# Kernel tuning notes

Hardware: AMD Instinct MI355X
Metric: run time of the kernel (lower is better)

## Reference

```python
import jax, jax.numpy as jnp
import numpy as np

B, S, D, H = 2, 2048, 1024, 16
DK = D // H  # 64
THETA = 10000.0


def setup_inputs() -> dict:
    key = jax.random.key(0)
    ks = jax.random.split(key, 5)
    std = float(np.sqrt(2.0 / (D + D)))
    x = jax.random.normal(ks[0], (B, S, D), dtype=jnp.float32)
    q_proj = jax.random.normal(ks[1], (D, D), dtype=jnp.float32) * std
    k_proj = jax.random.normal(ks[2], (D, D), dtype=jnp.float32) * std
    v_proj = jax.random.normal(ks[3], (D, D), dtype=jnp.float32) * std
    o_proj = jax.random.normal(ks[4], (D, D), dtype=jnp.float32) * std
    token_positions = jnp.arange(S, dtype=jnp.int32).reshape(1, S)
    return {"x": x, "token_positions": token_positions,
            "q_proj": q_proj, "k_proj": k_proj, "v_proj": v_proj, "o_proj": o_proj}


def _rope(t, pos):
    # t: [B, H, S, DK]; pos: [S]. Equivalent to multiplying by the block-diagonal
    # rotation matrix R[pos] in the source (interleaved 2x2 rotations).
    inv_freq = 1.0 / (THETA ** (2.0 * jnp.arange(DK // 2, dtype=jnp.float32) / DK))
    ang = pos.astype(jnp.float32)[:, None] * inv_freq[None, :]  # [S, DK/2]
    c, s = jnp.cos(ang), jnp.sin(ang)
    t0, t1 = t[..., 0::2], t[..., 1::2]
    out0 = c * t0 - s * t1
    out1 = s * t0 + c * t1
    return jnp.stack([out0, out1], axis=-1).reshape(t.shape)


def reference(x, token_positions, q_proj, k_proj, v_proj, o_proj):
    def split_heads(t):  # [B,S,D] -> [B,H,S,DK]
        return t.reshape(B, S, H, DK).transpose(0, 2, 1, 3)

    q = split_heads(jnp.einsum('bsd,ed->bse', x, q_proj))
    k = split_heads(jnp.einsum('bsd,ed->bse', x, k_proj))
    v = split_heads(jnp.einsum('bsd,ed->bse', x, v_proj))

    pos = token_positions[0]
    q = _rope(q, pos)
    k = _rope(k, pos)

    scores = jnp.einsum('bhqd,bhkd->bhqk', q, k) / jnp.sqrt(jnp.float32(DK))
    causal = jnp.tril(jnp.ones((S, S), dtype=bool))
    scores = jnp.where(causal, scores, -jnp.inf)

    # Faithful to source softmax: subtract the GLOBAL max (x.max()), then row-normalize.
    p = jnp.exp(scores - jnp.max(scores))
    p = p / jnp.sum(p, axis=-1, keepdims=True)

    attn = jnp.einsum('bhqk,bhkd->bhqd', p, v)
    attn = attn.transpose(0, 2, 1, 3).reshape(B, S, D)  # merge heads
    return jnp.einsum('bsd,ed->bse', attn, o_proj)
```

## Files before the change

kernel.cpp:

```cpp
#include <hip/hip_runtime.h>
#include <math.h>

#define B_  2
#define S_  2048
#define D_  1024
#define H_  16
#define DK_ 64
#define M_  (B_ * S_)

using u16 = unsigned short;
using u32 = unsigned int;
typedef __attribute__((ext_vector_type(8))) short  short8;
typedef __attribute__((ext_vector_type(4))) short  short4v;
typedef __attribute__((ext_vector_type(4))) float  float4v;
typedef __attribute__((ext_vector_type(4))) float  f32x4;
typedef __attribute__((ext_vector_type(4))) u32    u32x4;

__device__ __forceinline__ float bf2f(u16 h) {
  u32 u = ((u32)h) << 16;
  return __builtin_bit_cast(float, u);
}
__device__ __forceinline__ u16 f2bf(float f) {
  u32 u = __builtin_bit_cast(u32, f);
  u32 r = u + 0x7fffu + ((u >> 16) & 1u);
  return (u16)(r >> 16);
}

__device__ __forceinline__ void async16(const void* g, void* l) {
  __builtin_amdgcn_global_load_lds((const __attribute__((address_space(1))) void*)g,
                                   (__attribute__((address_space(3))) void*)l,
                                   16, 0, 0);
}

#define MFMA16(a, b, c) __builtin_amdgcn_mfma_f32_16x16x32_bf16((a), (b), (c), 0, 0, 0)

__device__ __forceinline__ void stc(u16* p, float v)   { *p = f2bf(v); }
__device__ __forceinline__ void stc(float* p, float v) { *p = v; }

#define XG_ (M_ * D_ / 4)
#define WG_ (D_ * D_ / 4)
__global__ __launch_bounds__(256) void cvt5_kernel(
    const float* __restrict__ x,  const float* __restrict__ wq,
    const float* __restrict__ wk, const float* __restrict__ wv,
    const float* __restrict__ wo, u16* __restrict__ Xb, u16* __restrict__ Wqb,
    u16* __restrict__ Wkb, u16* __restrict__ Wvb, u16* __restrict__ Wob) {
  int i = blockIdx.x * 256 + threadIdx.x;
  const float* s; u16* d; int off;
  if (i < XG_)                { s = x;  d = Xb;  off = i; }
  else if (i < XG_ + WG_)     { s = wq; d = Wqb; off = i - XG_; }
  else if (i < XG_ + 2 * WG_) { s = wk; d = Wkb; off = i - XG_ - WG_; }
  else if (i < XG_ + 3 * WG_) { s = wv; d = Wvb; off = i - XG_ - 2 * WG_; }
  else                        { s = wo; d = Wob; off = i - XG_ - 3 * WG_; }
  f32x4 v = ((const f32x4*)s)[off];
  short4v o;
  o[0] = (short)f2bf(v[0]); o[1] = (short)f2bf(v[1]);
  o[2] = (short)f2bf(v[2]); o[3] = (short)f2bf(v[3]);
  ((short4v*)d)[off] = o;
}

template <typename TC>
__device__ __forceinline__ void gemm_tile(const u16* __restrict__ A,
                                          const u16* __restrict__ Bw,
                                          TC* __restrict__ C,
                                          int K, int N, int m0, int n0) {
  __shared__ __align__(16) u16 As[128 * 32];
  __shared__ __align__(16) u16 Bs[128 * 32];
  const int tid  = threadIdx.x;
  const int lane = tid & 63;
  const int wave = tid >> 6;
  const int quad = lane >> 4;
  const int l15  = lane & 15;
  const int wm   = (wave >> 1) << 6;
  const int wn   = (wave & 1) << 6;

  float4v acc[4][4];
#pragma unroll
  for (int i = 0; i < 4; ++i)
#pragma unroll
    for (int j = 0; j < 4; ++j) acc[i][j] = (float4v){0.f, 0.f, 0.f, 0.f};

  for (int k0 = 0; k0 < K; k0 += 32) {
#pragma unroll
    for (int i = 0; i < 2; ++i) {
      const int cbase = i * 256 + wave * 64;
      const int c     = cbase + lane;
      async16(A  + (size_t)(m0 + (c >> 2)) * K + k0 + ((c & 3) << 3), As + cbase * 8);
      async16(Bw + (size_t)(n0 + (c >> 2)) * K + k0 + ((c & 3) << 3), Bs + cbase * 8);
    }
    __syncthreads();

    short8 af[4], bfr[4];
#pragma unroll
    for (int mi = 0; mi < 4; ++mi)
      af[mi] = *(const short8*)(As + (wm + mi * 16 + l15) * 32 + quad * 8);
#pragma unroll
    for (int ni = 0; ni < 4; ++ni)
      bfr[ni] = *(const short8*)(Bs + (wn + ni * 16 + l15) * 32 + quad * 8);
#pragma unroll
    for (int mi = 0; mi < 4; ++mi)
#pragma unroll
      for (int ni = 0; ni < 4; ++ni)
        acc[mi][ni] = MFMA16(af[mi], bfr[ni], acc[mi][ni]);
    __syncthreads();
  }

#pragma unroll
  for (int mi = 0; mi < 4; ++mi)
#pragma unroll
    for (int ni = 0; ni < 4; ++ni)
#pragma unroll
      for (int r = 0; r < 4; ++r) {
        const int row = m0 + wm + mi * 16 + quad * 4 + r;
        const int col = n0 + wn + ni * 16 + l15;
        stc(C + (size_t)row * N + col, acc[mi][ni][r]);
      }
}

__global__ __launch_bounds__(256) void gemm_qkv_kernel(
    const u16* __restrict__ X, const u16* __restrict__ Wq,
    const u16* __restrict__ Wk, const u16* __restrict__ Wv,
    u16* Qb, u16* Kb, u16* Vb) {
  const int mt  = blockIdx.x;
  const int nn  = blockIdx.y;
  const int sel = nn >> 3;
  const int nt  = nn & 7;
  const u16* Bw = (sel == 0) ? Wq : (sel == 1) ? Wk : Wv;
  u16*       C  = (sel == 0) ? Qb : (sel == 1) ? Kb : Vb;
  gemm_tile(X, Bw, C, D_, D_, mt * 128, nt * 128);
}

__global__ __launch_bounds__(256) void gemm_o_kernel(
    const u16* __restrict__ Ab, const u16* __restrict__ Wo, float* Out) {
  gemm_tile(Ab, Wo, Out, D_, D_, blockIdx.x * 128, blockIdx.y * 128);
}

__global__ __launch_bounds__(256) void rope_kernel(u16* __restrict__ Qb,
                                                   u16* __restrict__ Kb,
                                                   const void* __restrict__ posv) {
  const int t  = blockIdx.x * 256 + threadIdx.x;
  const int p4 = t & 7;
  const int h  = (t >> 3) & (H_ - 1);
  const int s  = (t >> 7) & (S_ - 1);
  const int b  = t >> 18;
  const int* p32 = (const int*)posv;
  const bool is64 = (p32[1] == 0 && p32[2] == 1);
  const int  ps   = is64 ? p32[2 * s] : p32[s];
  const float p   = (float)ps;
  const size_t base = (size_t)(b * S_ + s) * D_ + h * DK_ + p4 * 8;
  short8 qv = *(const short8*)(Qb + base);
  short8 kv = *(const short8*)(Kb + base);
  short8 qo, ko;
#pragma unroll
  for (int j = 0; j < 4; ++j) {
    const int i = p4 * 4 + j;
    const float freq = exp2f(-0.4152410118609203f * (float)i);
    float sn, cs;
    sincosf(p * freq, &sn, &cs);
    const float q0v = bf2f((u16)qv[2 * j]), q1v = bf2f((u16)qv[2 * j + 1]);
    qo[2 * j]     = (short)f2bf(0.125f * (cs * q0v - sn * q1v));
    qo[2 * j + 1] = (short)f2bf(0.125f * (sn * q0v + cs * q1v));
    const float k0v = bf2f((u16)kv[2 * j]), k1v = bf2f((u16)kv[2 * j + 1]);
    ko[2 * j]     = (short)f2bf(cs * k0v - sn * k1v);
    ko[2 * j + 1] = (short)f2bf(sn * k0v + cs * k1v);
  }
  *(short8*)(Qb + base) = qo;
  *(short8*)(Kb + base) = ko;
}

__global__ __launch_bounds__(256) void vtrans_kernel(const u16* __restrict__ Vb,
                                                     u16* __restrict__ Vt) {
  const int sblk = blockIdx.x;
  const int bh   = blockIdx.y;
  const int b = bh >> 4, h = bh & 15;
  const int t = threadIdx.x;
  const int s0 = sblk * 64;
  __shared__ __align__(16) u16 T[64 * 72];

  {
    const int srow = t >> 2;
    const int dseg = (t & 3) << 4;
    const u16* g = Vb + (size_t)(b * S_ + s0 + srow) * D_ + h * DK_ + dseg;
    *(short8*)(T + srow * 72 + dseg)     = *(const short8*)(g);
    *(short8*)(T + srow * 72 + dseg + 8) = *(const short8*)(g + 8);
  }
  __syncthreads();
  {
    const int dk   = t >> 2;
    const int sseg = (t & 3) << 4;
    short8 o0, o1;
#pragma unroll
    for (int j = 0; j < 8; ++j) {
      o0[j] = (short)T[(sseg + j) * 72 + dk];
      o1[j] = (short)T[(sseg + 8 + j) * 72 + dk];
    }
    u16* g = Vt + (size_t)(bh * DK_ + dk) * S_ + s0 + sseg;
    *(short8*)(g)     = o0;
    *(short8*)(g + 8) = o1;
  }
}

__global__ __launch_bounds__(128) void attn_kernel(const u16* __restrict__ Qb,
                                                   const u16* __restrict__ Kb,
                                                   const u16* __restrict__ Vt,
                                                   u16* __restrict__ Ob) {
  const int j5 = (blockIdx.x + blockIdx.y) & 31;
  const int r5 = j5 & 7, g5 = j5 >> 3;
  const int qt = (g5 == 0) ? r5 : (g5 == 1) ? r5 + 8 : (g5 == 2) ? 23 - r5 : 31 - r5;
  const int bh = blockIdx.y;
  const int b = bh >> 4, h = bh & 15;
  const int tid = threadIdx.x, lane = tid & 63, wave = tid >> 6;
  const int quad = lane >> 4, l15 = lane & 15;
  const int qw = qt * 64 + wave * 32;

  __shared__ __align__(16) u16 Kh[4][32 * 64];
  __shared__ __align__(16) u16 Vh[4][64 * 32];

  const u16* Kbh = Kb + (size_t)b * S_ * D_ + h * DK_;
  const u16* Vbh = Vt + (size_t)bh * DK_ * S_;

  auto stage = [&](int j) {
    const int sel = j & 3;
    const int k0  = j * 32;
#pragma unroll
    for (int i = 0; i < 2; ++i) {
      const int cb  = wave * 128 + i * 64;
      const int c   = cb + lane;
      const int row = c >> 3;
      const int ch  = (c & 7) ^ (row & 7);
      async16(Kbh + (size_t)(k0 + row) * D_ + ch * 8, &Kh[sel][cb * 8]);
    }
#pragma unroll
    for (int i = 0; i < 2; ++i) {
      const int cb = wave * 128 + i * 64;
      const int c  = cb + lane;
      const int rv = c >> 2;
      const int ch = (c & 3) ^ ((rv >> 1) & 3);
      async16(Vbh + (size_t)rv * S_ + k0 + ch * 8, &Vh[sel][cb * 8]);
    }
  };

  short8 qf[2][2];
#pragma unroll
  for (int rg = 0; rg < 2; ++rg) {
    const u16* qrow = Qb + (size_t)(b * S_ + qw + rg * 16 + l15) * D_ + h * DK_;
    qf[rg][0] = *(const short8*)(qrow + quad * 8);
    qf[rg][1] = *(const short8*)(qrow + 32 + quad * 8);
  }

  float4v oacc[2][4];
#pragma unroll
  for (int rg = 0; rg < 2; ++rg)
#pragma unroll
    for (int n2 = 0; n2 < 4; ++n2) oacc[rg][n2] = (float4v){0.f, 0.f, 0.f, 0.f};
  float lsum0 = 0.f, lsum1 = 0.f;

  const int NS = 2 * qt + 2;
  stage(0);
  stage(1);
  if (NS > 2) stage(2);

  for (int hs = 0; hs < NS; ++hs) {
    if (hs + 2 < NS)      asm volatile("s_waitcnt vmcnt(8)" ::: "memory");
    else if (hs + 1 < NS) asm volatile("s_waitcnt vmcnt(4)" ::: "memory");
    else                  asm volatile("s_waitcnt vmcnt(0)" ::: "memory");
    __builtin_amdgcn_s_barrier();
    asm volatile("" ::: "memory");
    if (hs + 3 < NS) stage(hs + 3);

    const int sel = hs & 3;
    const u16* ks = Kh[sel];
    const u16* vs = Vh[sel];

    float4v sc[2][2];
    __builtin_amdgcn_s_setprio(1);
#pragma unroll
    for (int ni = 0; ni < 2; ++ni) {
      const int kr = ni * 16 + l15;
      const int x  = kr & 7;
      const short8 kf0 = *(const short8*)(ks + kr * 64 + ((quad ^ x) << 3));
      const short8 kf1 = *(const short8*)(ks + kr * 64 + (((quad | 4) ^ x) << 3));
      float4v z = (float4v){0.f, 0.f, 0.f, 0.f};
      sc[0][ni] = MFMA16(kf1, qf[0][1], MFMA16(kf0, qf[0][0], z));
      sc[1][ni] = MFMA16(kf1, qf[1][1], MFMA16(kf0, qf[1][0], z));
    }
    __builtin_amdgcn_s_setprio(0);

    const int kbase = hs * 32;
    if (kbase + 31 > qw) {
#pragma unroll
      for (int rg = 0; rg < 2; ++rg) {
        const int qr = qw + rg * 16 + l15;
#pragma unroll
        for (int ni = 0; ni < 2; ++ni)
#pragma unroll
          for (int r = 0; r < 4; ++r) {
            const float e = __expf(sc[rg][ni][r]);
            sc[rg][ni][r] = (kbase + ni * 16 + quad * 4 + r > qr) ? 0.f : e;
          }
      }
    } else {
#pragma unroll
      for (int rg = 0; rg < 2; ++rg)
#pragma unroll
        for (int ni = 0; ni < 2; ++ni)
#pragma unroll
          for (int r = 0; r < 4; ++r) sc[rg][ni][r] = __expf(sc[rg][ni][r]);
    }

    short8 pfr[2];
#pragma unroll
    for (int rg = 0; rg < 2; ++rg) {
      u32 w0, w1, w2, w3;
      asm("v_cvt_pk_bf16_f32 %0, %1, %2" : "=v"(w0) : "v"(sc[rg][0][0]), "v"(sc[rg][0][1]));
      asm("v_cvt_pk_bf16_f32 %0, %1, %2" : "=v"(w1) : "v"(sc[rg][0][2]), "v"(sc[rg][0][3]));
      asm("v_cvt_pk_bf16_f32 %0, %1, %2" : "=v"(w2) : "v"(sc[rg][1][0]), "v"(sc[rg][1][1]));
      asm("v_cvt_pk_bf16_f32 %0, %1, %2" : "=v"(w3) : "v"(sc[rg][1][2]), "v"(sc[rg][1][3]));
      u32x4 ww = (u32x4){w0, w1, w2, w3};
      pfr[rg] = __builtin_bit_cast(short8, ww);
    }
#pragma unroll
    for (int ni = 0; ni < 2; ++ni)
#pragma unroll
      for (int r = 0; r < 4; ++r) {
        lsum0 += sc[0][ni][r];
        lsum1 += sc[1][ni][r];
      }

    __builtin_amdgcn_s_setprio(1);
#pragma unroll
    for (int n2 = 0; n2 < 4; ++n2) {
      const int vr = n2 * 16 + l15;
      const int sw = (vr >> 1) & 3;
      const short4v vlo = *(const short4v*)(vs + vr * 32 + (((quad >> 1) ^ sw) << 3) + ((quad & 1) << 2));
      const short4v vhi = *(const short4v*)(vs + vr * 32 + (((2 | (quad >> 1)) ^ sw) << 3) + ((quad & 1) << 2));
      short8 vf;
#pragma unroll
      for (int e = 0; e < 4; ++e) { vf[e] = vlo[e]; vf[e + 4] = vhi[e]; }
      oacc[0][n2] = MFMA16(pfr[0], vf, oacc[0][n2]);
      oacc[1][n2] = MFMA16(pfr[1], vf, oacc[1][n2]);
    }
    __builtin_amdgcn_s_setprio(0);
  }

  float ls[2] = {lsum0, lsum1};
#pragma unroll
  for (int rg = 0; rg < 2; ++rg) {
    float t = ls[rg];
    t += __shfl_xor(t, 16, 64);
    t += __shfl_xor(t, 32, 64);
    float rinv[4];
#pragma unroll
    for (int r = 0; r < 4; ++r) rinv[r] = 1.0f / __shfl(t, quad * 4 + r, 64);
#pragma unroll
    for (int n2 = 0; n2 < 4; ++n2)
#pragma unroll
      for (int r = 0; r < 4; ++r) {
        const int srow = qw + rg * 16 + quad * 4 + r;
        Ob[(size_t)(b * S_ + srow) * D_ + h * DK_ + n2 * 16 + l15] =
            f2bf(oacc[rg][n2][r] * rinv[r]);
      }
  }
}

extern "C" void kernel_launch(void* const* d_in, const int* in_sizes, int n_in,
                              void* d_out, int out_size, void* d_ws, size_t ws_size,
                              hipStream_t stream) {
  const float* x  = (const float*)d_in[0];
  const void*  tp = d_in[1];
  const float* wq = (const float*)d_in[2];
  const float* wk = (const float*)d_in[3];
  const float* wv = (const float*)d_in[4];
  const float* wo = (const float*)d_in[5];
  float* out = (float*)d_out;

  u16* Qb  = (u16*)d_ws;
  u16* Kb  = Qb + (size_t)M_ * D_;
  u16* Vb  = Kb + (size_t)M_ * D_;
  u16* Vt  = Vb + (size_t)M_ * D_;
  u16* Ab  = Vt + (size_t)M_ * D_;
  u16* Xb  = Ab;
  u16* Wqb = Ab + (size_t)M_ * D_;
  u16* Wkb = Wqb + (size_t)D_ * D_;
  u16* Wvb = Wkb + (size_t)D_ * D_;
  u16* Wob = Wvb + (size_t)D_ * D_;

  cvt5_kernel<<<dim3((XG_ + 4 * WG_) / 256), dim3(256), 0, stream>>>(
      x, wq, wk, wv, wo, Xb, Wqb, Wkb, Wvb, Wob);
  gemm_qkv_kernel<<<dim3(32, 24), dim3(256), 0, stream>>>(Xb, Wqb, Wkb, Wvb, Qb, Kb, Vb);
  rope_kernel<<<dim3((B_ * S_ * H_ * 8) / 256), dim3(256), 0, stream>>>(Qb, Kb, tp);
  vtrans_kernel<<<dim3(32, 32), dim3(256), 0, stream>>>(Vb, Vt);
  attn_kernel<<<dim3(32, 32), dim3(128), 0, stream>>>(Qb, Kb, Vt, Ab);
  gemm_o_kernel<<<dim3(32, 8), dim3(256), 0, stream>>>(Ab, Wob, out);
}
```

Measured before the change: 214.4 us.

## Restructure attention pipeline with precomputed offsets, unrolled steps and MFMA row sums

Several changes at once. The attention kernel now precomputes per-lane global and LDS offsets and advances pointers incrementally, and unrolls the loop four steps at a time with a constant buffer index. It also drops the V swizzle so each V fragment is a single short8 LDS read, and computes row sums with an extra MFMA against a ones vector instead of scalar adds and shuffles. The V transpose kernel permutes its key order to match, and the RoPE kernel computes sin/cos once per position into shared memory instead of per thread. Risks include LDS bank conflicts from the unswizzled V layout, and stages issued past NS loading out-of-range data that is never consumed.

After: 208.0 us. 3.0% less time.

```diff
diff --git a/kernel.cpp b/kernel.cpp
--- a/kernel.cpp
+++ b/kernel.cpp
@@ -137,15 +137,26 @@
 __global__ __launch_bounds__(256) void rope_kernel(u16* __restrict__ Qb,
                                                    u16* __restrict__ Kb,
                                                    const void* __restrict__ posv) {
-  const int t  = blockIdx.x * 256 + threadIdx.x;
+  const int tid = threadIdx.x;
+  const int t  = blockIdx.x * 256 + tid;
   const int p4 = t & 7;
   const int h  = (t >> 3) & (H_ - 1);
   const int s  = (t >> 7) & (S_ - 1);
   const int b  = t >> 18;
+  __shared__ float tabc[2][32], tabs[2][32];
   const int* p32 = (const int*)posv;
   const bool is64 = (p32[1] == 0 && p32[2] == 1);
-  const int  ps   = is64 ? p32[2 * s] : p32[s];
-  const float p   = (float)ps;
+  if (tid < 64) {
+    const int sl = tid >> 5, i = tid & 31;
+    const int sg = ((blockIdx.x * 2) & (S_ - 1)) + sl;
+    const int ps = is64 ? p32[2 * sg] : p32[sg];
+    const float freq = exp2f(-0.4152410118609203f * (float)i);
+    float sn, cs;
+    sincosf((float)ps * freq, &sn, &cs);
+    tabc[sl][i] = cs; tabs[sl][i] = sn;
+  }
+  __syncthreads();
+  const int sl = (tid >> 7) & 1;
   const size_t base = (size_t)(b * S_ + s) * D_ + h * DK_ + p4 * 8;
   short8 qv = *(const short8*)(Qb + base);
   short8 kv = *(const short8*)(Kb + base);
@@ -153,9 +164,7 @@
 #pragma unroll
   for (int j = 0; j < 4; ++j) {
     const int i = p4 * 4 + j;
-    const float freq = exp2f(-0.4152410118609203f * (float)i);
-    float sn, cs;
-    sincosf(p * freq, &sn, &cs);
+    const float cs = tabc[sl][i], sn = tabs[sl][i];
     const float q0v = bf2f((u16)qv[2 * j]), q1v = bf2f((u16)qv[2 * j + 1]);
     qo[2 * j]     = (short)f2bf(0.125f * (cs * q0v - sn * q1v));
     qo[2 * j + 1] = (short)f2bf(0.125f * (sn * q0v + cs * q1v));
@@ -189,9 +198,15 @@
     const int sseg = (t & 3) << 4;
     short8 o0, o1;
 #pragma unroll
-    for (int j = 0; j < 8; ++j) {
-      o0[j] = (short)T[(sseg + j) * 72 + dk];
-      o1[j] = (short)T[(sseg + 8 + j) * 72 + dk];
+    for (int jj = 0; jj < 8; ++jj) {
+      const int ss0 = sseg + jj;
+      const int ss1 = sseg + 8 + jj;
+      const int k0l = (((ss0 & 31) >> 3) << 2) + (((ss0 >> 2) & 1) << 4) +
+                      (ss0 & 3) + (ss0 & 32);
+      const int k1l = (((ss1 & 31) >> 3) << 2) + (((ss1 >> 2) & 1) << 4) +
+                      (ss1 & 3) + (ss1 & 32);
+      o0[jj] = (short)T[k0l * 72 + dk];
+      o1[jj] = (short)T[k1l * 72 + dk];
     }
     u16* g = Vt + (size_t)(bh * DK_ + dk) * S_ + s0 + sseg;
     *(short8*)(g)     = o0;
@@ -215,29 +230,35 @@
   __shared__ __align__(16) u16 Kh[4][32 * 64];
   __shared__ __align__(16) u16 Vh[4][64 * 32];
 
-  const u16* Kbh = Kb + (size_t)b * S_ * D_ + h * DK_;
-  const u16* Vbh = Vt + (size_t)bh * DK_ * S_;
-
-  auto stage = [&](int j) {
-    const int sel = j & 3;
-    const int k0  = j * 32;
-#pragma unroll
-    for (int i = 0; i < 2; ++i) {
-      const int cb  = wave * 128 + i * 64;
-      const int c   = cb + lane;
-      const int row = c >> 3;
-      const int ch  = (c & 7) ^ (row & 7);
-      async16(Kbh + (size_t)(k0 + row) * D_ + ch * 8, &Kh[sel][cb * 8]);
-    }
+  int koffb[2], voffb[2];
+#pragma unroll
+  for (int i = 0; i < 2; ++i) {
+    const int c  = wave * 128 + i * 64 + lane;
+    const int kr = c >> 3;
+    const int kj = (c & 7) ^ (kr & 7);
+    koffb[i] = kr * (D_ * 2) + kj * 16;
+    const int vdk = c >> 2;
+    const int vj  = c & 3;
+    voffb[i] = vdk * (S_ * 2) + vj * 16;
+  }
+  const char* kp = (const char*)(Kb + (size_t)b * S_ * D_ + h * DK_);
+  const char* vp = (const char*)(Vt + (size_t)bh * DK_ * S_);
+
+  auto stage = [&](int sel) {
 #pragma unroll
     for (int i = 0; i < 2; ++i) {
       const int cb = wave * 128 + i * 64;
-      const int c  = cb + lane;
-      const int rv = c >> 2;
-      const int ch = (c & 3) ^ ((rv >> 1) & 3);
-      async16(Vbh + (size_t)rv * S_ + k0 + ch * 8, &Vh[sel][cb * 8]);
+      async16(kp + koffb[i], &Kh[sel][cb * 8]);
+      async16(vp + voffb[i], &Vh[sel][cb * 8]);
     }
+    kp += 32 * D_ * 2;
+    vp += 64;
   };
+
+  const int x7   = l15 & 7;
+  const int krd0 = l15 * 64 + ((quad ^ x7) << 3);
+  const int krd1 = l15 * 64 + (((quad + 4) ^ x7) << 3);
+  const int vrd  = l15 * 32 + (quad << 3);
 
   short8 qf[2][2];
 #pragma unroll
@@ -246,111 +267,103 @@
     qf[rg][0] = *(const short8*)(qrow + quad * 8);
     qf[rg][1] = *(const short8*)(qrow + 32 + quad * 8);
   }
+  asm volatile("s_waitcnt vmcnt(0)" ::: "memory");
+
+  short8 ones;
+#pragma unroll
+  for (int j = 0; j < 8; ++j) ones[j] = (short)0x3F80;
 
   float4v oacc[2][4];
 #pragma unroll
   for (int rg = 0; rg < 2; ++rg)
 #pragma unroll
     for (int n2 = 0; n2 < 4; ++n2) oacc[rg][n2] = (float4v){0.f, 0.f, 0.f, 0.f};
-  float lsum0 = 0.f, lsum1 = 0.f;
+  float4v lacc[2] = {(float4v){0.f, 0.f, 0.f, 0.f}, (float4v){0.f, 0.f, 0.f, 0.f}};
 
   const int NS = 2 * qt + 2;
-  stage(0);
-  stage(1);
-  if (NS > 2) stage(2);
-
-  for (int hs = 0; hs < NS; ++hs) {
-    if (hs + 2 < NS)      asm volatile("s_waitcnt vmcnt(8)" ::: "memory");
-    else if (hs + 1 < NS) asm volatile("s_waitcnt vmcnt(4)" ::: "memory");
-    else                  asm volatile("s_waitcnt vmcnt(0)" ::: "memory");
-    __builtin_amdgcn_s_barrier();
-    asm volatile("" ::: "memory");
-    if (hs + 3 < NS) stage(hs + 3);
-
-    const int sel = hs & 3;
-    const u16* ks = Kh[sel];
-    const u16* vs = Vh[sel];
-
-    float4v sc[2][2];
-    __builtin_amdgcn_s_setprio(1);
-#pragma unroll
-    for (int ni = 0; ni < 2; ++ni) {
-      const int kr = ni * 16 + l15;
-      const int x  = kr & 7;
-      const short8 kf0 = *(const short8*)(ks + kr * 64 + ((quad ^ x) << 3));
-      const short8 kf1 = *(const short8*)(ks + kr * 64 + (((quad | 4) ^ x) << 3));
-      float4v z = (float4v){0.f, 0.f, 0.f, 0.f};
-      sc[0][ni] = MFMA16(kf1, qf[0][1], MFMA16(kf0, qf[0][0], z));
-      sc[1][ni] = MFMA16(kf1, qf[1][1], MFMA16(kf0, qf[1][0], z));
-    }
-    __builtin_amdgcn_s_setprio(0);
-
-    const int kbase = hs * 32;
-    if (kbase + 31 > qw) {
-#pragma unroll
-      for (int rg = 0; rg < 2; ++rg) {
-        const int qr = qw + rg * 16 + l15;
-#pragma unroll
-        for (int ni = 0; ni < 2; ++ni)
-#pragma unroll
-          for (int r = 0; r < 4; ++r) {
-            const float e = __expf(sc[rg][ni][r]);
-            sc[rg][ni][r] = (kbase + ni * 16 + quad * 4 + r > qr) ? 0.f : e;
-          }
-      }
-    } else {
-#pragma unroll
-      for (int rg = 0; rg < 2; ++rg)
-#pragma unroll
-        for (int ni = 0; ni < 2; ++ni)
-#pragma unroll
-          for (int r = 0; r < 4; ++r) sc[rg][ni][r] = __expf(sc[rg][ni][r]);
-    }
-
-    short8 pfr[2];
-#pragma unroll
-    for (int rg = 0; rg < 2; ++rg) {
-      u32 w0, w1, w2, w3;
-      asm("v_cvt_pk_bf16_f32 %0, %1, %2" : "=v"(w0) : "v"(sc[rg][0][0]), "v"(sc[rg][0][1]));
-      asm("v_cvt_pk_bf16_f32 %0, %1, %2" : "=v"(w1) : "v"(sc[rg][0][2]), "v"(sc[rg][0][3]));
-      asm("v_cvt_pk_bf16_f32 %0, %1, %2" : "=v"(w2) : "v"(sc[rg][1][0]), "v"(sc[rg][1][1]));
-      asm("v_cvt_pk_bf16_f32 %0, %1, %2" : "=v"(w3) : "v"(sc[rg][1][2]), "v"(sc[rg][1][3]));
-      u32x4 ww = (u32x4){w0, w1, w2, w3};
-      pfr[rg] = __builtin_bit_cast(short8, ww);
-    }
-#pragma unroll
-    for (int ni = 0; ni < 2; ++ni)
-#pragma unroll
-      for (int r = 0; r < 4; ++r) {
-        lsum0 += sc[0][ni][r];
-        lsum1 += sc[1][ni][r];
-      }
-
-    __builtin_amdgcn_s_setprio(1);
-#pragma unroll
-    for (int n2 = 0; n2 < 4; ++n2) {
-      const int vr = n2 * 16 + l15;
-      const int sw = (vr >> 1) & 3;
-      const short4v vlo = *(const short4v*)(vs + vr * 32 + (((quad >> 1) ^ sw) << 3) + ((quad & 1) << 2));
-      const short4v vhi = *(const short4v*)(vs + vr * 32 + (((2 | (quad >> 1)) ^ sw) << 3) + ((quad & 1) << 2));
-      short8 vf;
-#pragma unroll
-      for (int e = 0; e < 4; ++e) { vf[e] = vlo[e]; vf[e + 4] = vhi[e]; }
-      oacc[0][n2] = MFMA16(pfr[0], vf, oacc[0][n2]);
-      oacc[1][n2] = MFMA16(pfr[1], vf, oacc[1][n2]);
-    }
-    __builtin_amdgcn_s_setprio(0);
-  }
-
-  float ls[2] = {lsum0, lsum1};
+  int kb = 0;
+  stage(0); stage(1); stage(2);
+
+#define ATT_STEP(SEL)                                                          \
+  {                                                                            \
+    asm volatile("s_waitcnt vmcnt(8)" ::: "memory");                           \
+    __builtin_amdgcn_s_barrier();                                              \
+    asm volatile("" ::: "memory");                                             \
+    stage(((SEL) + 3) & 3);                                                    \
+    const u16* ks = &Kh[(SEL)][0];                                             \
+    const u16* vs = &Vh[(SEL)][0];                                             \
+    float4v sc[2][2];                                                          \
+    __builtin_amdgcn_s_setprio(1);                                             \
+    _Pragma("unroll")                                                          \
+    for (int ni = 0; ni < 2; ++ni) {                                           \
+      const short8 kf0 = *(const short8*)(ks + krd0 + ni * 1024);              \
+      const short8 kf1 = *(const short8*)(ks + krd1 + ni * 1024);              \
+      float4v z = (float4v){0.f, 0.f, 0.f, 0.f};                               \
+      sc[0][ni] = MFMA16(kf1, qf[0][1], MFMA16(kf0, qf[0][0], z));             \
+      sc[1][ni] = MFMA16(kf1, qf[1][1], MFMA16(kf0, qf[1][0], z));             \
+    }                                                                          \
+    __builtin_amdgcn_s_setprio(0);                                             \
+    if (kb + 31 > qw) {                                                        \
+      _Pragma("unroll")                                                        \
+      for (int rg = 0; rg < 2; ++rg) {                                         \
+        const int qr = qw + rg * 16 + l15;                                     \
+        _Pragma("unroll")                                                      \
+        for (int ni = 0; ni < 2; ++ni)                                         \
+          _Pragma("unroll")                                                    \
+          for (int r = 0; r < 4; ++r) {                                        \
+            const float e = __expf(sc[rg][ni][r]);                             \
+            sc[rg][ni][r] = (kb + ni * 16 + quad * 4 + r > qr) ? 0.f : e;      \
+          }                                                                    \
+      }                                                                        \
+    } else {                                                                   \
+      _Pragma("unroll")                                                        \
+      for (int rg = 0; rg < 2; ++rg)                                           \
+        _Pragma("unroll")                                                      \
+        for (int ni = 0; ni < 2; ++ni)                                         \
+          _Pragma("unroll")                                                    \
+          for (int r = 0; r < 4; ++r) sc[rg][ni][r] = __expf(sc[rg][ni][r]);   \
+    }                                                                          \
+    short8 pfr[2];                                                             \
+    _Pragma("unroll")                                                          \
+    for (int rg = 0; rg < 2; ++rg) {                                           \
+      u32 w0, w1, w2, w3;                                                      \
+      asm("v_cvt_pk_bf16_f32 %0, %1, %2" : "=v"(w0) : "v"(sc[rg][0][0]), "v"(sc[rg][0][1])); \
+      asm("v_cvt_pk_bf16_f32 %0, %1, %2" : "=v"(w1) : "v"(sc[rg][0][2]), "v"(sc[rg][0][3])); \
+      asm("v_cvt_pk_bf16_f32 %0, %1, %2" : "=v"(w2) : "v"(sc[rg][1][0]), "v"(sc[rg][1][1])); \
+      asm("v_cvt_pk_bf16_f32 %0, %1, %2" : "=v"(w3) : "v"(sc[rg][1][2]), "v"(sc[rg][1][3])); \
+      u32x4 ww = (u32x4){w0, w1, w2, w3};                                      \
+      pfr[rg] = __builtin_bit_cast(short8, ww);                                \
+    }                                                                          \
+    __builtin_amdgcn_s_setprio(1);                                             \
+    lacc[0] = MFMA16(pfr[0], ones, lacc[0]);                                   \
+    lacc[1] = MFMA16(pfr[1], ones, lacc[1]);                                   \
+    _Pragma("unroll")                                                          \
+    for (int n2 = 0; n2 < 4; ++n2) {                                           \
+      const short8 vf = *(const short8*)(vs + vrd + n2 * 512);                 \
+      oacc[0][n2] = MFMA16(pfr[0], vf, oacc[0][n2]);                           \
+      oacc[1][n2] = MFMA16(pfr[1], vf, oacc[1][n2]);                           \
+    }                                                                          \
+    __builtin_amdgcn_s_setprio(0);                                             \
+    kb += 32;                                                                  \
+  }
+
+  int hs = 0;
+  while (hs + 4 <= NS) {
+    ATT_STEP(0) ATT_STEP(1) ATT_STEP(2) ATT_STEP(3)
+    hs += 4;
+  }
+  if (hs < NS) {
+    ATT_STEP(0) ATT_STEP(1)
+  }
+  asm volatile("s_waitcnt vmcnt(0)" ::: "memory");
+
+#undef ATT_STEP
+
 #pragma unroll
   for (int rg = 0; rg < 2; ++rg) {
-    float t = ls[rg];
-    t += __shfl_xor(t, 16, 64);
-    t += __shfl_xor(t, 32, 64);
     float rinv[4];
 #pragma unroll
-    for (int r = 0; r < 4; ++r) rinv[r] = 1.0f / __shfl(t, quad * 4 + r, 64);
+    for (int r = 0; r < 4; ++r) rinv[r] = 1.0f / lacc[rg][r];
 #pragma unroll
     for (int n2 = 0; n2 < 4; ++n2)
 #pragma unroll
```

## Split attention key range across wave pairs, use MFMA row sums, precompute RoPE table

Applied to the files above, without the earlier changes.

The attention kernel now runs 256 threads per block. Each pair of waves shares a 32-row query slice and splits every 64-key tile between them, and the two partial outputs and row sums are combined through shared memory at the end. Row sums are now computed with an MFMA against a vector of ones, replacing scalar adds and shuffles. The K/V staging moves to a double-buffered 64-key layout with a new swizzle, and vtrans permutes key order to match the new V fragment read. RoPE computes a per-block sin/cos table in shared memory instead of calling sincos in every thread. This trades pipeline depth (vmcnt(0) each iteration) and extra combine traffic for more waves and fewer VALU ops.

After: 180.0 us. 1.19x faster.

```diff
diff --git a/kernel.cpp b/kernel.cpp
--- a/kernel.cpp
+++ b/kernel.cpp
@@ -137,15 +137,26 @@
 __global__ __launch_bounds__(256) void rope_kernel(u16* __restrict__ Qb,
                                                    u16* __restrict__ Kb,
                                                    const void* __restrict__ posv) {
-  const int t  = blockIdx.x * 256 + threadIdx.x;
+  const int tid = threadIdx.x;
+  const int t  = blockIdx.x * 256 + tid;
   const int p4 = t & 7;
   const int h  = (t >> 3) & (H_ - 1);
   const int s  = (t >> 7) & (S_ - 1);
   const int b  = t >> 18;
+  __shared__ float tabc[2][32], tabs[2][32];
   const int* p32 = (const int*)posv;
   const bool is64 = (p32[1] == 0 && p32[2] == 1);
-  const int  ps   = is64 ? p32[2 * s] : p32[s];
-  const float p   = (float)ps;
+  if (tid < 64) {
+    const int sl = tid >> 5, i = tid & 31;
+    const int sg = ((blockIdx.x * 2) & (S_ - 1)) + sl;
+    const int ps = is64 ? p32[2 * sg] : p32[sg];
+    const float freq = exp2f(-0.4152410118609203f * (float)i);
+    float sn, cs;
+    sincosf((float)ps * freq, &sn, &cs);
+    tabc[sl][i] = cs; tabs[sl][i] = sn;
+  }
+  __syncthreads();
+  const int sl = (tid >> 7) & 1;
   const size_t base = (size_t)(b * S_ + s) * D_ + h * DK_ + p4 * 8;
   short8 qv = *(const short8*)(Qb + base);
   short8 kv = *(const short8*)(Kb + base);
@@ -153,9 +164,7 @@
 #pragma unroll
   for (int j = 0; j < 4; ++j) {
     const int i = p4 * 4 + j;
-    const float freq = exp2f(-0.4152410118609203f * (float)i);
-    float sn, cs;
-    sincosf(p * freq, &sn, &cs);
+    const float cs = tabc[sl][i], sn = tabs[sl][i];
     const float q0v = bf2f((u16)qv[2 * j]), q1v = bf2f((u16)qv[2 * j + 1]);
     qo[2 * j]     = (short)f2bf(0.125f * (cs * q0v - sn * q1v));
     qo[2 * j + 1] = (short)f2bf(0.125f * (sn * q0v + cs * q1v));
@@ -189,9 +198,15 @@
     const int sseg = (t & 3) << 4;
     short8 o0, o1;
 #pragma unroll
-    for (int j = 0; j < 8; ++j) {
-      o0[j] = (short)T[(sseg + j) * 72 + dk];
-      o1[j] = (short)T[(sseg + 8 + j) * 72 + dk];
+    for (int jj = 0; jj < 8; ++jj) {
+      const int ss0 = sseg + jj;
+      const int ss1 = sseg + 8 + jj;
+      const int k0l = (((ss0 & 31) >> 3) << 2) + (((ss0 >> 2) & 1) << 4) +
+                      (ss0 & 3) + (ss0 & 32);
+      const int k1l = (((ss1 & 31) >> 3) << 2) + (((ss1 >> 2) & 1) << 4) +
+                      (ss1 & 3) + (ss1 & 32);
+      o0[jj] = (short)T[k0l * 72 + dk];
+      o1[jj] = (short)T[k1l * 72 + dk];
     }
     u16* g = Vt + (size_t)(bh * DK_ + dk) * S_ + s0 + sseg;
     *(short8*)(g)     = o0;
@@ -199,45 +214,52 @@
   }
 }
 
-__global__ __launch_bounds__(128) void attn_kernel(const u16* __restrict__ Qb,
-                                                   const u16* __restrict__ Kb,
-                                                   const u16* __restrict__ Vt,
-                                                   u16* __restrict__ Ob) {
+__global__ __launch_bounds__(256, 4) void attn_kernel(const u16* __restrict__ Qb,
+                                                      const u16* __restrict__ Kb,
+                                                      const u16* __restrict__ Vt,
+                                                      u16* __restrict__ Ob) {
   const int j5 = (blockIdx.x + blockIdx.y) & 31;
   const int r5 = j5 & 7, g5 = j5 >> 3;
   const int qt = (g5 == 0) ? r5 : (g5 == 1) ? r5 + 8 : (g5 == 2) ? 23 - r5 : 31 - r5;
   const int bh = blockIdx.y;
   const int b = bh >> 4, h = bh & 15;
   const int tid = threadIdx.x, lane = tid & 63, wave = tid >> 6;
+  const int qh = wave >> 1, kh = wave & 1;
   const int quad = lane >> 4, l15 = lane & 15;
-  const int qw = qt * 64 + wave * 32;
-
-  __shared__ __align__(16) u16 Kh[4][32 * 64];
-  __shared__ __align__(16) u16 Vh[4][64 * 32];
-
-  const u16* Kbh = Kb + (size_t)b * S_ * D_ + h * DK_;
-  const u16* Vbh = Vt + (size_t)bh * DK_ * S_;
-
-  auto stage = [&](int j) {
-    const int sel = j & 3;
-    const int k0  = j * 32;
-#pragma unroll
-    for (int i = 0; i < 2; ++i) {
-      const int cb  = wave * 128 + i * 64;
-      const int c   = cb + lane;
-      const int row = c >> 3;
-      const int ch  = (c & 7) ^ (row & 7);
-      async16(Kbh + (size_t)(k0 + row) * D_ + ch * 8, &Kh[sel][cb * 8]);
-    }
+  const int qw = qt * 64 + qh * 32;
+
+  __shared__ __align__(16) u16 SM[2][2][64 * 64];
+
+  const char* kp = (const char*)(Kb + (size_t)b * S_ * D_ + h * DK_);
+  const char* vp = (const char*)(Vt + (size_t)bh * DK_ * S_);
+
+  int koffb[2], voffb[2];
+#pragma unroll
+  for (int i = 0; i < 2; ++i) {
+    const int c  = wave * 128 + i * 64 + lane;
+    const int kr = c >> 3;
+    const int kj = (c & 7) ^ (kr & 7);
+    koffb[i] = kr * (D_ * 2) + kj * 16;
+    const int vdk = c >> 3;
+    const int vj  = (c & 7) ^ (vdk & 7);
+    voffb[i] = vdk * (S_ * 2) + vj * 16;
+  }
+
+  auto stage = [&](int sel) {
 #pragma unroll
     for (int i = 0; i < 2; ++i) {
       const int cb = wave * 128 + i * 64;
-      const int c  = cb + lane;
-      const int rv = c >> 2;
-      const int ch = (c & 3) ^ ((rv >> 1) & 3);
-      async16(Vbh + (size_t)rv * S_ + k0 + ch * 8, &Vh[sel][cb * 8]);
-    }
+      async16(kp + koffb[i], &SM[0][sel][cb * 8]);
+      async16(vp + voffb[i], &SM[1][sel][cb * 8]);
+    }
+    kp += 64 * D_ * 2;
+    vp += 128;
   };
+
+  const int x7   = l15 & 7;
+  const int krd0 = (kh * 32 + l15) * 64 + ((quad ^ x7) << 3);
+  const int krd1 = (kh * 32 + l15) * 64 + (((quad + 4) ^ x7) << 3);
+  const int vrd  = l15 * 64 + (((kh * 4 + quad) ^ x7) << 3);
 
   short8 qf[2][2];
 #pragma unroll
@@ -247,46 +269,43 @@
     qf[rg][1] = *(const short8*)(qrow + 32 + quad * 8);
   }
 
+  short8 ones;
+#pragma unroll
+  for (int j = 0; j < 8; ++j) ones[j] = (short)0x3F80;
+
   float4v oacc[2][4];
 #pragma unroll
   for (int rg = 0; rg < 2; ++rg)
 #pragma unroll
     for (int n2 = 0; n2 < 4; ++n2) oacc[rg][n2] = (float4v){0.f, 0.f, 0.f, 0.f};
-  float lsum0 = 0.f, lsum1 = 0.f;
-
-  const int NS = 2 * qt + 2;
+  float4v lacc[2] = {(float4v){0.f, 0.f, 0.f, 0.f}, (float4v){0.f, 0.f, 0.f, 0.f}};
+
+  const int NS = qt + 1;
   stage(0);
-  stage(1);
-  if (NS > 2) stage(2);
-
-  for (int hs = 0; hs < NS; ++hs) {
-    if (hs + 2 < NS)      asm volatile("s_waitcnt vmcnt(8)" ::: "memory");
-    else if (hs + 1 < NS) asm volatile("s_waitcnt vmcnt(4)" ::: "memory");
-    else                  asm volatile("s_waitcnt vmcnt(0)" ::: "memory");
+
+  for (int j = 0; j < NS; ++j) {
+    asm volatile("s_waitcnt vmcnt(0)" ::: "memory");
     __builtin_amdgcn_s_barrier();
     asm volatile("" ::: "memory");
-    if (hs + 3 < NS) stage(hs + 3);
-
-    const int sel = hs & 3;
-    const u16* ks = Kh[sel];
-    const u16* vs = Vh[sel];
+    if (j + 1 < NS) stage((j + 1) & 1);
+
+    const u16* ks = &SM[0][j & 1][0];
+    const u16* vs = &SM[1][j & 1][0];
 
     float4v sc[2][2];
     __builtin_amdgcn_s_setprio(1);
 #pragma unroll
     for (int ni = 0; ni < 2; ++ni) {
-      const int kr = ni * 16 + l15;
-      const int x  = kr & 7;
-      const short8 kf0 = *(const short8*)(ks + kr * 64 + ((quad ^ x) << 3));
-      const short8 kf1 = *(const short8*)(ks + kr * 64 + (((quad | 4) ^ x) << 3));
+      const short8 kf0 = *(const short8*)(ks + krd0 + ni * 1024);
+      const short8 kf1 = *(const short8*)(ks + krd1 + ni * 1024);
       float4v z = (float4v){0.f, 0.f, 0.f, 0.f};
       sc[0][ni] = MFMA16(kf1, qf[0][1], MFMA16(kf0, qf[0][0], z));
       sc[1][ni] = MFMA16(kf1, qf[1][1], MFMA16(kf0, qf[1][0], z));
     }
     __builtin_amdgcn_s_setprio(0);
 
-    const int kbase = hs * 32;
-    if (kbase + 31 > qw) {
+    const int kb = j * 64 + kh * 32;
+    if (kb + 31 > qw) {
 #pragma unroll
       for (int rg = 0; rg < 2; ++rg) {
         const int qr = qw + rg * 16 + l15;
@@ -295,7 +314,7 @@
 #pragma unroll
           for (int r = 0; r < 4; ++r) {
             const float e = __expf(sc[rg][ni][r]);
-            sc[rg][ni][r] = (kbase + ni * 16 + quad * 4 + r > qr) ? 0.f : e;
+            sc[rg][ni][r] = (kb + ni * 16 + quad * 4 + r > qr) ? 0.f : e;
           }
       }
     } else {
@@ -318,47 +337,51 @@
       u32x4 ww = (u32x4){w0, w1, w2, w3};
       pfr[rg] = __builtin_bit_cast(short8, ww);
     }
-#pragma unroll
-    for (int ni = 0; ni < 2; ++ni)
-#pragma unroll
-      for (int r = 0; r < 4; ++r) {
-        lsum0 += sc[0][ni][r];
-        lsum1 += sc[1][ni][r];
-      }
 
     __builtin_amdgcn_s_setprio(1);
+    lacc[0] = MFMA16(pfr[0], ones, lacc[0]);
+    lacc[1] = MFMA16(pfr[1], ones, lacc[1]);
 #pragma unroll
     for (int n2 = 0; n2 < 4; ++n2) {
-      const int vr = n2 * 16 + l15;
-      const int sw = (vr >> 1) & 3;
-      const short4v vlo = *(const short4v*)(vs + vr * 32 + (((quad >> 1) ^ sw) << 3) + ((quad & 1) << 2));
-      const short4v vhi = *(const short4v*)(vs + vr * 32 + (((2 | (quad >> 1)) ^ sw) << 3) + ((quad & 1) << 2));
-      short8 vf;
-#pragma unroll
-      for (int e = 0; e < 4; ++e) { vf[e] = vlo[e]; vf[e + 4] = vhi[e]; }
+      const short8 vf = *(const short8*)(vs + vrd + n2 * 1024);
       oacc[0][n2] = MFMA16(pfr[0], vf, oacc[0][n2]);
       oacc[1][n2] = MFMA16(pfr[1], vf, oacc[1][n2]);
     }
     __builtin_amdgcn_s_setprio(0);
   }
 
-  float ls[2] = {lsum0, lsum1};
-#pragma unroll
-  for (int rg = 0; rg < 2; ++rg) {
-    float t = ls[rg];
-    t += __shfl_xor(t, 16, 64);
-    t += __shfl_xor(t, 32, 64);
-    float rinv[4];
-#pragma unroll
-    for (int r = 0; r < 4; ++r) rinv[r] = 1.0f / __shfl(t, quad * 4 + r, 64);
-#pragma unroll
-    for (int n2 = 0; n2 < 4; ++n2)
-#pragma unroll
-      for (int r = 0; r < 4; ++r) {
-        const int srow = qw + rg * 16 + quad * 4 + r;
-        Ob[(size_t)(b * S_ + srow) * D_ + h * DK_ + n2 * 16 + l15] =
-            f2bf(oacc[rg][n2][r] * rinv[r]);
-      }
+  __syncthreads();
+  float* comb = (float*)(void*)&SM[0][0][0];
+  if (kh == 1) {
+    float* cw = comb + (size_t)(qh * 64 + lane) * 41;
+#pragma unroll
+    for (int rg = 0; rg < 2; ++rg) {
+#pragma unroll
+      for (int n2 = 0; n2 < 4; ++n2)
+#pragma unroll
+        for (int r = 0; r < 4; ++r) cw[rg * 16 + n2 * 4 + r] = oacc[rg][n2][r];
+#pragma unroll
+      for (int r = 0; r < 4; ++r) cw[32 + rg * 4 + r] = lacc[rg][r];
+    }
+  }
+  __syncthreads();
+  if (kh == 0) {
+    const float* cw = comb + (size_t)(qh * 64 + lane) * 41;
+#pragma unroll
+    for (int rg = 0; rg < 2; ++rg) {
+      float rinv[4];
+#pragma unroll
+      for (int r = 0; r < 4; ++r)
+        rinv[r] = 1.0f / (lacc[rg][r] + cw[32 + rg * 4 + r]);
+#pragma unroll
+      for (int n2 = 0; n2 < 4; ++n2)
+#pragma unroll
+        for (int r = 0; r < 4; ++r) {
+          const int srow = qw + rg * 16 + quad * 4 + r;
+          Ob[(size_t)(b * S_ + srow) * D_ + h * DK_ + n2 * 16 + l15] =
+              f2bf((oacc[rg][n2][r] + cw[rg * 16 + n2 * 4 + r]) * rinv[r]);
+        }
+    }
   }
 }
 
@@ -389,6 +412,6 @@
   gemm_qkv_kernel<<<dim3(32, 24), dim3(256), 0, stream>>>(Xb, Wqb, Wkb, Wvb, Qb, Kb, Vb);
   rope_kernel<<<dim3((B_ * S_ * H_ * 8) / 256), dim3(256), 0, stream>>>(Qb, Kb, tp);
   vtrans_kernel<<<dim3(32, 32), dim3(256), 0, stream>>>(Vb, Vt);
-  attn_kernel<<<dim3(32, 32), dim3(128), 0, stream>>>(Qb, Kb, Vt, Ab);
+  attn_kernel<<<dim3(32, 32), dim3(256), 0, stream>>>(Qb, Kb, Vt, Ab);
   gemm_o_kernel<<<dim3(32, 8), dim3(256), 0, stream>>>(Ab, Wob, out);
 }
```
